# Optimization experiments

Hardware: AMD Instinct MI355X
Metric: run time of the kernel (lower is better)

The kernel has to match this reference:

```python
import jax, jax.numpy as jnp
import numpy as np

N_NODES = 50000
N_EDGES = 1600000


def _seg_softmax(e, seg, n):
    # numerically-stable softmax over edges grouped by destination node
    m = jax.ops.segment_max(e, seg, num_segments=n)
    ex = jnp.exp(e - m[seg])
    s = jax.ops.segment_sum(ex, seg, num_segments=n)
    return ex / s[seg]


def setup_inputs() -> dict:
    key = jax.random.key(0)
    ks = jax.random.split(key, 16)
    IN, OUT, ED = 64, 32, 8
    inp = {
        'x': jax.random.normal(ks[0], (N_NODES, IN), jnp.float32),
        'ex': jax.random.normal(ks[1], (N_EDGES, ED), jnp.float32),
        'src': jax.random.randint(ks[2], (N_EDGES,), 0, N_NODES),
        'dst': jax.random.randint(ks[3], (N_EDGES,), 0, N_NODES),
        'W_fc': jax.random.normal(ks[4], (OUT, IN), jnp.float32) * 0.1,
        'b_fc': jax.random.normal(ks[5], (OUT,), jnp.float32) * 0.1,
        'W_att': jax.random.normal(ks[6], (1, 2 * OUT + ED), jnp.float32) * 0.1,
        'b_att': jax.random.normal(ks[7], (1,), jnp.float32) * 0.1,
        'W_edge': jax.random.normal(ks[8], (OUT, ED), jnp.float32) * 0.1,
        'b_edge': jax.random.normal(ks[9], (OUT,), jnp.float32) * 0.1,
        'W_eatt': jax.random.normal(ks[10], (ED, ED), jnp.float32) * 0.1,
        'b_eatt': jax.random.normal(ks[11], (ED,), jnp.float32) * 0.1,
        'W_q': jax.random.normal(ks[12], (OUT, OUT), jnp.float32) * 0.1,
        'b_q': jax.random.normal(ks[13], (OUT,), jnp.float32) * 0.1,
        'W_s': jax.random.normal(ks[14], (OUT, OUT), jnp.float32) * 0.1,
        'b_s': jax.random.normal(ks[15], (OUT,), jnp.float32) * 0.1,
    }
    return inp


def reference(x, ex, src, dst, W_fc, b_fc, W_att, b_att, W_edge, b_edge,
              W_eatt, b_eatt, W_q, b_q, W_s, b_s):
    n = x.shape[0]
    # node transform (fc; batch norm disabled in config)
    z = x @ W_fc.T + b_fc                      # [N, OUT]
    z_src = z[src]                             # [E, OUT]
    z_dst = z[dst]                             # [E, OUT]
    # edge transform for attention score
    ex_t = ex @ W_eatt.T + b_eatt              # [E, ED]
    # edge-dependent attention logit + leaky_relu(0.2)
    z2 = jnp.concatenate([z_src, z_dst, ex_t], axis=1)  # [E, 2*OUT+ED]
    a = z2 @ W_att.T + b_att                   # [E, 1]
    e = jnp.where(a >= 0, a, 0.2 * a)
    # edge feature aggregation transform
    ez = ex @ W_edge.T + b_edge                # [E, OUT]
    # similar_node branch: pointwise conv1d == linear; per-edge dot product
    q = z_src @ W_q.T + b_q                    # query(src)
    s = z_dst @ W_s.T + b_s                    # support(dst)
    es = jnp.sum(q * s, axis=1, keepdims=True)  # [E, 1]
    # edge-softmax over incoming edges of each destination node
    alpha = _seg_softmax(e, dst, n)            # [E, 1]
    similar = _seg_softmax(es, dst, n)         # [E, 1]
    h_att = jax.ops.segment_sum(alpha * z_src, dst, num_segments=n)    # [N, OUT]
    h2 = jax.ops.segment_sum(similar * z_src, dst, num_segments=n)     # [N, OUT]
    h = h_att * h2
    # attention-weighted edge feature aggregation
    h = h + jax.ops.segment_sum(alpha * ez, dst, num_segments=n)
    return h, alpha
```

## Files before the change

kernel.cpp:

```cpp
#include <hip/hip_runtime.h>
#include <hip/hip_fp16.h>

#define OUTF 32
#define INF 64
#define EDF 8
#define BSH 8
#define BN  (1 << BSH)
#define NBK 256
#define EPB 4096

__global__ __launch_bounds__(256) void prep_kernel(
    const float* __restrict__ x,
    const float* __restrict__ W_fc, const float* __restrict__ b_fc,
    const float* __restrict__ W_q,  const float* __restrict__ b_q,
    const float* __restrict__ W_s,  const float* __restrict__ b_s,
    const float* __restrict__ W_att,
    __half* __restrict__ z16, float* __restrict__ t,
    float* __restrict__ c_es,
    float* __restrict__ att_s, float* __restrict__ att_d,
    int* __restrict__ bhist, int n_nodes)
{
    int i = blockIdx.x * 256 + threadIdx.x;
    if (i < NBK) bhist[i] = 0;
    if (i >= n_nodes) return;
    int n = i;

    float xl[INF];
    for (int k = 0; k < INF; k++) xl[k] = x[(size_t)n * INF + k];

    float zl[OUTF];
    float a1 = 0.f, a2 = 0.f;
    for (int o = 0; o < OUTF; o++) {
        float acc = b_fc[o];
        for (int k = 0; k < INF; k++) acc += xl[k] * W_fc[o * INF + k];
        zl[o] = acc;
        z16[(size_t)n * OUTF + o] = __float2half(acc);
        a1 += acc * W_att[o];
        a2 += acc * W_att[OUTF + o];
    }
    att_s[n] = a1;
    att_d[n] = a2;

    float sl[OUTF];
    float ces = 0.f;
    for (int o = 0; o < OUTF; o++) {
        float as = b_s[o];
        for (int k = 0; k < OUTF; k++) as += zl[k] * W_s[o * OUTF + k];
        sl[o] = as;
        ces += b_q[o] * as;
    }
    c_es[n] = ces;
    for (int k = 0; k < OUTF; k++) {
        float tv = 0.f;
        for (int o = 0; o < OUTF; o++) tv += W_q[o * OUTF + k] * sl[o];
        t[(size_t)n * OUTF + k] = tv;
    }
}

__global__ __launch_bounds__(1024) void bhist_kernel(
    const int* __restrict__ didx, int* __restrict__ bhist, int E)
{
    __shared__ int cnt[NBK];
    int tid = threadIdx.x;
    if (tid < NBK) cnt[tid] = 0;
    __syncthreads();
    int e0 = blockIdx.x * EPB;
    #pragma unroll 4
    for (int k = 0; k < 4; k++) {
        int e = e0 + k * 1024 + tid;
        if (e < E) atomicAdd(&cnt[didx[e] >> BSH], 1);
    }
    __syncthreads();
    if (tid < NBK && cnt[tid]) atomicAdd(&bhist[tid], cnt[tid]);
}

__global__ __launch_bounds__(256) void bscan_kernel(
    const int* __restrict__ bhist, int* __restrict__ bbase,
    int* __restrict__ bcursor, int nbk)
{
    __shared__ int sh[256];
    int t = threadIdx.x;
    int v = (t < nbk) ? bhist[t] : 0;
    sh[t] = v;
    __syncthreads();
    for (int st = 1; st < 256; st <<= 1) {
        int tv = (t >= st) ? sh[t - st] : 0;
        __syncthreads();
        sh[t] += tv;
        __syncthreads();
    }
    if (t < nbk) {
        int excl = sh[t] - v;
        bbase[t] = excl;
        bcursor[t] = excl;
        if (t == nbk - 1) bbase[nbk] = sh[t];
    }
}

__device__ __forceinline__ unsigned pack2h(float a, float b) {
    __half2 h = __floats2half2_rn(a, b);
    return *(unsigned*)&h;
}

__global__ __launch_bounds__(1024) void bin_kernel(
    const int* __restrict__ sidx, const int* __restrict__ didx,
    const float* __restrict__ ex,
    const float* __restrict__ att_s, const float* __restrict__ att_d,
    const float* __restrict__ W_att, const float* __restrict__ b_att,
    const float* __restrict__ W_eatt, const float* __restrict__ b_eatt,
    int* __restrict__ bcursor, int* __restrict__ stage_meta,
    uint4* __restrict__ stage_ex, float* __restrict__ alpha_out, int E)
{
    __shared__ int cnt[NBK];
    __shared__ int gbase[NBK];
    __shared__ float v3[EDF];
    __shared__ float ccs;
    int tid = threadIdx.x;
    if (tid < NBK) cnt[tid] = 0;
    if (tid < EDF) {
        float a = 0.f;
        for (int j = 0; j < EDF; j++) a += W_att[2 * OUTF + j] * W_eatt[j * EDF + tid];
        v3[tid] = a;
    }
    if (tid == 0) {
        float a = b_att[0];
        for (int j = 0; j < EDF; j++) a += W_att[2 * OUTF + j] * b_eatt[j];
        ccs = a;
    }
    __syncthreads();
    int e0 = blockIdx.x * EPB;
    int srcv[4], dstv[4], rankv[4];
    #pragma unroll 4
    for (int k = 0; k < 4; k++) {
        int e = e0 + k * 1024 + tid;
        if (e < E) {
            srcv[k] = sidx[e]; dstv[k] = didx[e];
            rankv[k] = atomicAdd(&cnt[dstv[k] >> BSH], 1);
        } else srcv[k] = -1;
    }
    __syncthreads();
    if (tid < NBK && cnt[tid]) gbase[tid] = atomicAdd(&bcursor[tid], cnt[tid]);
    __syncthreads();
    #pragma unroll 4
    for (int k = 0; k < 4; k++) {
        if (srcv[k] >= 0) {
            int e = e0 + k * 1024 + tid;
            int b = dstv[k] >> BSH;
            int pos = gbase[b] + rankv[k];
            stage_meta[pos] = srcv[k] | ((dstv[k] & (BN - 1)) << 16);
            const float4* exr = (const float4*)(ex + (size_t)e * EDF);
            float4 a = exr[0], c = exr[1];
            stage_ex[pos] = make_uint4(pack2h(a.x, a.y), pack2h(a.z, a.w),
                                       pack2h(c.x, c.y), pack2h(c.z, c.w));
            float anum = att_s[srcv[k]] + att_d[dstv[k]] + ccs
                       + a.x * v3[0] + a.y * v3[1] + a.z * v3[2] + a.w * v3[3]
                       + c.x * v3[4] + c.y * v3[5] + c.z * v3[6] + c.w * v3[7];
            float el = (anum >= 0.f) ? anum : 0.2f * anum;
            alpha_out[e] = __expf(el);
        }
    }
}

__global__ __launch_bounds__(1024) void place_kernel(
    const int* __restrict__ bbase, const int* __restrict__ stage_meta,
    int* __restrict__ csr_pos, int* __restrict__ nodeStart,
    int* __restrict__ nodeCnt, int N)
{
    __shared__ int cnt[BN], excl[BN], cur[BN], scan[BN];
    int tid = threadIdx.x;
    int b = blockIdx.x;
    int nodeBase = b << BSH;
    int beg = bbase[b], end = bbase[b + 1];

    if (tid < BN) cnt[tid] = 0;
    __syncthreads();
    for (int j = beg + tid; j < end; j += 1024)
        atomicAdd(&cnt[(stage_meta[j] >> 16) & (BN - 1)], 1);
    __syncthreads();
    if (tid < BN) scan[tid] = cnt[tid];
    __syncthreads();
    for (int st = 1; st < BN; st <<= 1) {
        int v = (tid < BN && tid >= st) ? scan[tid - st] : 0;
        __syncthreads();
        if (tid < BN) scan[tid] += v;
        __syncthreads();
    }
    if (tid < BN) {
        excl[tid] = scan[tid] - cnt[tid];
        cur[tid] = excl[tid];
    }
    __syncthreads();
    for (int j = beg + tid; j < end; j += 1024) {
        int dl = (stage_meta[j] >> 16) & (BN - 1);
        int pos = atomicAdd(&cur[dl], 1);
        csr_pos[beg + pos] = j;
    }
    __syncthreads();
    if (tid < BN) {
        int n = nodeBase + tid;
        if (n < N) {
            nodeStart[n] = beg + excl[tid];
            nodeCnt[n] = cnt[tid];
        }
    }
}

__device__ __forceinline__ float4 loadHalf4(const __half* p) {
    uint2 raw = *(const uint2*)p;
    __half2 h01 = *reinterpret_cast<__half2*>(&raw.x);
    __half2 h23 = *reinterpret_cast<__half2*>(&raw.y);
    float2 f01 = __half22float2(h01);
    float2 f23 = __half22float2(h23);
    return make_float4(f01.x, f01.y, f23.x, f23.y);
}
__device__ __forceinline__ float2 unp2(unsigned u) {
    __half2 h = *reinterpret_cast<__half2*>(&u);
    return __half22float2(h);
}

__global__ __launch_bounds__(256) void agg_kernel(
    const int* __restrict__ nodeStart, const int* __restrict__ nodeCnt,
    const int* __restrict__ csr_pos,
    const int* __restrict__ stage_meta, const uint4* __restrict__ stage_ex,
    const float* __restrict__ att_d, const float* __restrict__ c_es,
    const __half* __restrict__ z16, const float* __restrict__ t,
    const float* __restrict__ W_att, const float* __restrict__ b_att,
    const float* __restrict__ W_eatt, const float* __restrict__ b_eatt,
    const float* __restrict__ W_edge, const float* __restrict__ b_edge,
    float* __restrict__ h_out, float* __restrict__ invS_out, int N)
{
    __shared__ float sv3[EDF];
    __shared__ float ccs;
    __shared__ float sWedge[OUTF * EDF];
    __shared__ float sbedge[OUTF];
    int tid = threadIdx.x;
    if (tid < EDF) {
        float a = 0.f;
        for (int j = 0; j < EDF; j++) a += W_att[2 * OUTF + j] * W_eatt[j * EDF + tid];
        sv3[tid] = a;
    }
    if (tid == 0) {
        float a = b_att[0];
        for (int j = 0; j < EDF; j++) a += W_att[2 * OUTF + j] * b_eatt[j];
        ccs = a;
    }
    if (tid < OUTF * EDF) sWedge[tid] = W_edge[tid];
    if (tid < OUTF) sbedge[tid] = b_edge[tid];
    __syncthreads();

    int wave = blockIdx.x * 4 + (tid >> 6);
    if (wave >= N) return;
    int lane = tid & 63;
    int g = lane >> 3;
    int l = lane & 7;
    int n = wave;
    int beg = nodeStart[n], ec = nodeCnt[n];

    float4 t4  = *(const float4*)(t + (size_t)n * OUTF + l * 4);
    float4 wa4 = *(const float4*)(W_att + l * 4);
    float4 v34 = (l < 2) ? *(const float4*)(sv3 + l * 4)
                         : make_float4(0.f, 0.f, 0.f, 0.f);
    float attc = att_d[n] + ccs;
    float cesn = c_es[n];

    float S = 0.f, Spe = 0.f;
    float4 U1 = make_float4(0.f, 0.f, 0.f, 0.f);
    float4 U2 = U1, Uax = U1;

    for (int e0 = 0; e0 < ec; e0 += 16) {
        int jA = e0 + g;
        bool vA = jA < ec;
        int idxA = csr_pos[beg + (vA ? jA : 0)];
        int jB = e0 + 8 + g;
        bool vB = jB < ec;
        int idxB = csr_pos[beg + (vB ? jB : 0)];

        int srcA = stage_meta[idxA] & 0xFFFF;
        int srcB = stage_meta[idxB] & 0xFFFF;
        uint4 ejA = stage_ex[idxA];
        uint4 ejB = stage_ex[idxB];

        float4 zA = loadHalf4(z16 + (size_t)srcA * OUTF + l * 4);
        float4 zB = loadHalf4(z16 + (size_t)srcB * OUTF + l * 4);
        float4 eA, eB;
        if (l == 0) { float2 p0 = unp2(ejA.x), p1 = unp2(ejA.y); eA = make_float4(p0.x, p0.y, p1.x, p1.y);
                      float2 q0 = unp2(ejB.x), q1 = unp2(ejB.y); eB = make_float4(q0.x, q0.y, q1.x, q1.y); }
        else if (l == 1) { float2 p0 = unp2(ejA.z), p1 = unp2(ejA.w); eA = make_float4(p0.x, p0.y, p1.x, p1.y);
                           float2 q0 = unp2(ejB.z), q1 = unp2(ejB.w); eB = make_float4(q0.x, q0.y, q1.x, q1.y); }
        else { eA = make_float4(0.f, 0.f, 0.f, 0.f); eB = eA; }

        float rA = zA.x * t4.x + zA.y * t4.y + zA.z * t4.z + zA.w * t4.w;
        float mA = zA.x * wa4.x + zA.y * wa4.y + zA.z * wa4.z + zA.w * wa4.w
                 + eA.x * v34.x + eA.y * v34.y + eA.z * v34.z + eA.w * v34.w;
        float rB = zB.x * t4.x + zB.y * t4.y + zB.z * t4.z + zB.w * t4.w;
        float mB = zB.x * wa4.x + zB.y * wa4.y + zB.z * wa4.z + zB.w * wa4.w
                 + eB.x * v34.x + eB.y * v34.y + eB.z * v34.z + eB.w * v34.w;
        #pragma unroll
        for (int m = 4; m >= 1; m >>= 1) {
            rA += __shfl_xor(rA, m);
            mA += __shfl_xor(mA, m);
            rB += __shfl_xor(rB, m);
            mB += __shfl_xor(mB, m);
        }
        float aA = mA + attc;
        float aB = mB + attc;
        float pA  = vA ? __expf(aA >= 0.f ? aA : 0.2f * aA) : 0.f;
        float peA = vA ? __expf(rA + cesn) : 0.f;
        float pB  = vB ? __expf(aB >= 0.f ? aB : 0.2f * aB) : 0.f;
        float peB = vB ? __expf(rB + cesn) : 0.f;

        S += pA + pB; Spe += peA + peB;
        U1.x += pA * zA.x + pB * zB.x;  U1.y += pA * zA.y + pB * zB.y;
        U1.z += pA * zA.z + pB * zB.z;  U1.w += pA * zA.w + pB * zB.w;
        U2.x += peA * zA.x + peB * zB.x; U2.y += peA * zA.y + peB * zB.y;
        U2.z += peA * zA.z + peB * zB.z; U2.w += peA * zA.w + peB * zB.w;
        Uax.x += pA * eA.x + pB * eB.x; Uax.y += pA * eA.y + pB * eB.y;
        Uax.z += pA * eA.z + pB * eB.z; Uax.w += pA * eA.w + pB * eB.w;
    }

    #pragma unroll
    for (int m = 8; m <= 32; m <<= 1) {
        S   += __shfl_xor(S, m);
        Spe += __shfl_xor(Spe, m);
        U1.x += __shfl_xor(U1.x, m); U1.y += __shfl_xor(U1.y, m);
        U1.z += __shfl_xor(U1.z, m); U1.w += __shfl_xor(U1.w, m);
        U2.x += __shfl_xor(U2.x, m); U2.y += __shfl_xor(U2.y, m);
        U2.z += __shfl_xor(U2.z, m); U2.w += __shfl_xor(U2.w, m);
        Uax.x += __shfl_xor(Uax.x, m); Uax.y += __shfl_xor(Uax.y, m);
        Uax.z += __shfl_xor(Uax.z, m); Uax.w += __shfl_xor(Uax.w, m);
    }

    float invS = 0.f;
    float4 h4 = make_float4(0.f, 0.f, 0.f, 0.f);
    if (ec > 0) {
        invS = 1.f / S;
        float invSpe = 1.f / Spe;
        float ax[EDF];
        ax[0] = __shfl(Uax.x, 0); ax[1] = __shfl(Uax.y, 0);
        ax[2] = __shfl(Uax.z, 0); ax[3] = __shfl(Uax.w, 0);
        ax[4] = __shfl(Uax.x, 1); ax[5] = __shfl(Uax.y, 1);
        ax[6] = __shfl(Uax.z, 1); ax[7] = __shfl(Uax.w, 1);
        #pragma unroll
        for (int j = 0; j < 4; j++) {
            int c = l * 4 + j;
            float hagg = sbedge[c];
            #pragma unroll
            for (int k = 0; k < EDF; k++)
                hagg += sWedge[c * EDF + k] * (ax[k] * invS);
            float hatt = ((j == 0) ? U1.x : (j == 1) ? U1.y : (j == 2) ? U1.z : U1.w) * invS;
            float h2   = ((j == 0) ? U2.x : (j == 1) ? U2.y : (j == 2) ? U2.z : U2.w) * invSpe;
            ((float*)&h4)[j] = hatt * h2 + hagg;
        }
    }
    if (lane < 8) {
        *(float4*)(h_out + (size_t)n * OUTF + l * 4) = h4;
        if (lane == 0) invS_out[n] = invS;
    }
}

__global__ __launch_bounds__(256) void scale_kernel(
    const int* __restrict__ didx, const float* __restrict__ invS,
    float* __restrict__ alpha_out, int E)
{
    int e = blockIdx.x * 256 + threadIdx.x;
    if (e < E) alpha_out[e] *= invS[didx[e]];
}

extern "C" void kernel_launch(void* const* d_in, const int* in_sizes, int n_in,
                              void* d_out, int out_size, void* d_ws, size_t ws_size,
                              hipStream_t stream) {
    const float* x      = (const float*)d_in[0];
    const float* ex     = (const float*)d_in[1];
    const int*   sidx   = (const int*)d_in[2];
    const int*   didx   = (const int*)d_in[3];
    const float* W_fc   = (const float*)d_in[4];
    const float* b_fc   = (const float*)d_in[5];
    const float* W_att  = (const float*)d_in[6];
    const float* b_att  = (const float*)d_in[7];
    const float* W_edge = (const float*)d_in[8];
    const float* b_edge = (const float*)d_in[9];
    const float* W_eatt = (const float*)d_in[10];
    const float* b_eatt = (const float*)d_in[11];
    const float* W_q    = (const float*)d_in[12];
    const float* b_q    = (const float*)d_in[13];
    const float* W_s    = (const float*)d_in[14];
    const float* b_s    = (const float*)d_in[15];

    int N = in_sizes[0] / INF;
    int E = in_sizes[2];
    int N32 = N * OUTF;
    int nbk = (N + BN - 1) >> BSH;

    float* h_out     = (float*)d_out;
    float* alpha_out = h_out + N32;

    float*  base    = (float*)d_ws;
    float*  att_s   = base;
    float*  att_d   = att_s + N;
    float*  invS    = att_d + N;
    float*  c_es    = invS + N;
    __half* z16     = (__half*)(c_es + N);
    float*  t       = (float*)(z16 + (size_t)N * OUTF);
    int*    nodeStart = (int*)(t + N32);
    int*    nodeCnt   = nodeStart + N;
    int*    stage_meta = nodeCnt + N;
    uint4*  stage_ex   = (uint4*)(stage_meta + E);
    int*    csr_pos = (int*)(stage_ex + E);
    int*    bhist   = csr_pos + E;
    int*    bbase   = bhist + NBK;
    int*    bcursor = bbase + NBK + 1;

    prep_kernel<<<(N + 255) / 256, 256, 0, stream>>>(
        x, W_fc, b_fc, W_q, b_q, W_s, b_s, W_att,
        z16, t, c_es, att_s, att_d, bhist, N);

    int nbC = (E + EPB - 1) / EPB;
    bhist_kernel<<<nbC, 1024, 0, stream>>>(didx, bhist, E);
    bscan_kernel<<<1, 256, 0, stream>>>(bhist, bbase, bcursor, nbk);
    bin_kernel<<<nbC, 1024, 0, stream>>>(sidx, didx, ex, att_s, att_d,
                                         W_att, b_att, W_eatt, b_eatt,
                                         bcursor, stage_meta, stage_ex,
                                         alpha_out, E);
    place_kernel<<<nbk, 1024, 0, stream>>>(bbase, stage_meta, csr_pos,
                                           nodeStart, nodeCnt, N);

    int nbAgg = (N + 3) / 4;
    agg_kernel<<<nbAgg, 256, 0, stream>>>(
        nodeStart, nodeCnt, csr_pos, stage_meta, stage_ex,
        att_d, c_es, z16, t,
        W_att, b_att, W_eatt, b_eatt, W_edge, b_edge,
        h_out, invS, N);

    int nbE = (E + 255) / 256;
    scale_kernel<<<nbE, 256, 0, stream>>>(didx, invS, alpha_out, E);
}
```

Before: 202.3 us.

## Locally sort edges by bucket in shared memory before scattering to staging

The binning kernel now builds a shared-memory permutation that groups each block's edges by destination bucket, using a prefix scan of the bucket counts. Consecutive threads then write consecutive staging positions, so the scattered stage_meta and stage_ex stores become mostly contiguous per bucket. The cost is a 16KB shared array, an extra scan with several barriers, and reading src/dst/ex and writing alpha in permuted order, which makes those accesses less coalesced.

```diff
diff --git a/kernel.cpp b/kernel.cpp
--- a/kernel.cpp
+++ b/kernel.cpp
@@ -112,7 +112,9 @@
     uint4* __restrict__ stage_ex, float* __restrict__ alpha_out, int E)
 {
     __shared__ int cnt[NBK];
+    __shared__ int loffE[NBK];
     __shared__ int gbase[NBK];
+    __shared__ int perm[EPB];
     __shared__ float v3[EDF];
     __shared__ float ccs;
     int tid = threadIdx.x;
@@ -128,36 +130,64 @@
         ccs = a;
     }
     __syncthreads();
+
     int e0 = blockIdx.x * EPB;
-    int srcv[4], dstv[4], rankv[4];
+    int nLoc = E - e0; if (nLoc > EPB) nLoc = EPB;
+
+    int bk[4], rk[4];
     #pragma unroll 4
     for (int k = 0; k < 4; k++) {
-        int e = e0 + k * 1024 + tid;
-        if (e < E) {
-            srcv[k] = sidx[e]; dstv[k] = didx[e];
-            rankv[k] = atomicAdd(&cnt[dstv[k] >> BSH], 1);
-        } else srcv[k] = -1;
-    }
-    __syncthreads();
-    if (tid < NBK && cnt[tid]) gbase[tid] = atomicAdd(&bcursor[tid], cnt[tid]);
-    __syncthreads();
+        int le = k * 1024 + tid;
+        if (le < nLoc) {
+            int b = didx[e0 + le] >> BSH;
+            bk[k] = b;
+            rk[k] = atomicAdd(&cnt[b], 1);
+        } else bk[k] = -1;
+    }
+    __syncthreads();
+
+    __shared__ int scan[NBK];
+    if (tid < NBK) scan[tid] = cnt[tid];
+    __syncthreads();
+    for (int st = 1; st < NBK; st <<= 1) {
+        int v = (tid < NBK && tid >= st) ? scan[tid - st] : 0;
+        __syncthreads();
+        if (tid < NBK) scan[tid] += v;
+        __syncthreads();
+    }
+    if (tid < NBK) {
+        loffE[tid] = scan[tid] - cnt[tid];
+        gbase[tid] = cnt[tid] ? atomicAdd(&bcursor[tid], cnt[tid]) : 0;
+    }
+    __syncthreads();
+
     #pragma unroll 4
     for (int k = 0; k < 4; k++) {
-        if (srcv[k] >= 0) {
-            int e = e0 + k * 1024 + tid;
-            int b = dstv[k] >> BSH;
-            int pos = gbase[b] + rankv[k];
-            stage_meta[pos] = srcv[k] | ((dstv[k] & (BN - 1)) << 16);
-            const float4* exr = (const float4*)(ex + (size_t)e * EDF);
-            float4 a = exr[0], c = exr[1];
-            stage_ex[pos] = make_uint4(pack2h(a.x, a.y), pack2h(a.z, a.w),
-                                       pack2h(c.x, c.y), pack2h(c.z, c.w));
-            float anum = att_s[srcv[k]] + att_d[dstv[k]] + ccs
-                       + a.x * v3[0] + a.y * v3[1] + a.z * v3[2] + a.w * v3[3]
-                       + c.x * v3[4] + c.y * v3[5] + c.z * v3[6] + c.w * v3[7];
-            float el = (anum >= 0.f) ? anum : 0.2f * anum;
-            alpha_out[e] = __expf(el);
+        if (bk[k] >= 0) {
+            int le = k * 1024 + tid;
+            perm[loffE[bk[k]] + rk[k]] = le | (bk[k] << 12);
         }
+    }
+    __syncthreads();
+
+    for (int j = tid; j < nLoc; j += 1024) {
+        int v = perm[j];
+        int le = v & 4095;
+        int b  = (v >> 12) & 255;
+        int e  = e0 + le;
+        int pos = gbase[b] + (j - loffE[b]);
+
+        int src = sidx[e], dst = didx[e];
+        stage_meta[pos] = src | ((dst & (BN - 1)) << 16);
+        const float4* exr = (const float4*)(ex + (size_t)e * EDF);
+        float4 a = exr[0], c = exr[1];
+        stage_ex[pos] = make_uint4(pack2h(a.x, a.y), pack2h(a.z, a.w),
+                                   pack2h(c.x, c.y), pack2h(c.z, c.w));
+        float anum = att_s[src] + att_d[dst] + ccs
+                   + a.x * v3[0] + a.y * v3[1] + a.z * v3[2] + a.w * v3[3]
+                   + c.x * v3[4] + c.y * v3[5] + c.z * v3[6] + c.w * v3[7];
+        float el = (anum >= 0.f) ? anum : 0.2f * anum;
+        alpha_out[e] = __expf(el);
     }
 }
 
```

Result: slower. 224.8 us (+11.1%).
